# Kernel optimization log

Measured on AMD Instinct MI355X. Metric: run time of the kernel, lower is better.

## Reference

```python
import jax, jax.numpy as jnp
import numpy as np


def _conv_nchw(x, w, strides):
    # F.conv2d with padding=0 -> VALID, NCHW / OIHW layout
    return jax.lax.conv_general_dilated(
        x, w, window_strides=tuple(strides), padding="VALID",
        dimension_numbers=("NCHW", "OIHW", "NCHW"))


def setup_inputs() -> dict:
    key = jax.random.key(0)
    kx, kw, kb = jax.random.split(key, 3)
    # scale so values span the full int8 range and all 8 bit-planes are active
    x = jax.random.normal(kx, (64, 64, 56, 56), dtype=jnp.float32) * 60.0
    weight = jax.random.normal(kw, (128, 64, 3, 3), dtype=jnp.float32) * 0.05
    bias = jax.random.normal(kb, (128,), dtype=jnp.float32)
    return {"x": x, "weight": weight, "bias": bias}


def reference(x, weight, bias):
    strides = (1, 1)
    # clamp to int8 range and cast (torch.clamp + .type(torch.int8))
    xi = jnp.clip(x, -128, 127).astype(jnp.int8)
    y = jnp.zeros((), dtype=weight.dtype)
    for i in range(8):
        # arithmetic shift on signed int8, matching torch semantics
        bit = ((xi >> i) & 1).astype(weight.dtype)
        yi = jnp.clip(_conv_nchw(bit, weight, strides), -1024, 1023)
        scale = jnp.asarray(-128.0 if i == 7 else float(2 ** i), dtype=weight.dtype)
        y = y + yi * scale
    y = y + bias.reshape(1, -1, 1, 1)
    return y
```

## Files before the change

### kernel.cpp

```cpp
#include <hip/hip_runtime.h>
#include <stdint.h>

typedef unsigned short u16;
typedef __attribute__((ext_vector_type(8))) __bf16 bf16x8;
typedef __attribute__((ext_vector_type(4))) float f32x4;

#define N_IMG 64
#define C_IN  64
#define HW_IN 3136
#define W_IN  56
#define C_OUT 128
#define OH    54
#define OW    54
#define SPI   2916
#define KTOT  576
#define M_TOTAL (N_IMG*SPI)

typedef __attribute__((address_space(3))) unsigned int lds_uint;
typedef __attribute__((address_space(1))) unsigned int gbl_uint;

__device__ __forceinline__ void load16_to_lds(const u16* g, u16* l) {
  __builtin_amdgcn_global_load_lds((const gbl_uint*)g, (lds_uint*)l, 16, 0, 0);
}

__device__ inline u16 f32_bf16_rne(float f) {
  unsigned u = __float_as_uint(f);
  u = (u + 0x7FFFu + ((u >> 16) & 1u)) >> 16;
  return (u16)u;
}

__global__ void convert_w(const float* __restrict__ w, u16* __restrict__ wtT) {
  int o = blockIdx.x * 256 + threadIdx.x;
  if (o >= C_OUT * KTOT) return;
  int co = o / KTOT;
  int k  = o - co * KTOT;
  int t  = k >> 6;
  int ci = k & 63;
  wtT[o] = f32_bf16_rne(w[co * KTOT + ci * 9 + t]);
}

__global__ __launch_bounds__(256) void convert_x(const float* __restrict__ x,
                                                 u16* __restrict__ xt) {
  __shared__ u16 tile[64][66];
  int n  = blockIdx.y;
  int s0 = blockIdx.x * 64;
  int tx = threadIdx.x, ty = threadIdx.y;
  const float* xp = x + (size_t)n * C_IN * HW_IN;
  #pragma unroll
  for (int i = ty; i < 64; i += 4) {
    float v = xp[i * HW_IN + s0 + tx];
    v = fminf(fmaxf(v, -128.f), 127.f);
    int iv = (int)v;
    tile[i][tx] = f32_bf16_rne((float)iv);
  }
  __syncthreads();
  u16* op = xt + (size_t)n * HW_IN * C_IN;
  #pragma unroll
  for (int i = ty; i < 64; i += 4) {
    op[(size_t)(s0 + i) * C_IN + tx] = tile[tx][i];
  }
}

__global__ __launch_bounds__(256) void conv_gemm(
    const u16* __restrict__ xt, const u16* __restrict__ wtT,
    const float* __restrict__ bias, float* __restrict__ y)
{
  __shared__ u16 sP[128 * 64];
  __shared__ u16 sW[128 * 64];

  int tid  = threadIdx.x;
  int wv   = tid >> 6;
  int lane = tid & 63;
  int ln   = lane & 15;
  int q    = lane >> 4;
  int wy   = wv >> 1;
  int wx   = wv & 1;

  int blk_sp0 = blockIdx.x * 128;

  int r8 = lane >> 3;
  int cg = lane & 7;
  int scol = (cg ^ r8) * 8;

  int pix_off[4], wt_off[4];
  #pragma unroll
  for (int j = 0; j < 4; j++) {
    int srow = wv * 32 + j * 8 + r8;
    int p   = blk_sp0 + srow;
    int img = p / SPI;  int rem = p - img * SPI;
    int oh  = rem / OW; int ow  = rem - oh * OW;
    pix_off[j] = (img * HW_IN + oh * W_IN + ow) * C_IN + scol;
    wt_off[j]  = srow * KTOT + scol;
  }

  f32x4 acc[4][4];
  #pragma unroll
  for (int mt = 0; mt < 4; mt++)
    #pragma unroll
    for (int nt = 0; nt < 4; nt++)
      acc[mt][nt] = (f32x4){0.f, 0.f, 0.f, 0.f};

  int wrow[4], prow[4];
  #pragma unroll
  for (int i = 0; i < 4; i++) {
    wrow[i] = (wy * 64 + i * 16 + ln) * 64;
    prow[i] = (wx * 64 + i * 16 + ln) * 64;
  }
  int l7 = ln & 7;

  #pragma unroll
  for (int kc = 0; kc < 9; kc++) {
    int kh = kc / 3, kw = kc - kh * 3;
    int xoff = (kh * W_IN + kw) * C_IN;

    __syncthreads();
    #pragma unroll
    for (int j = 0; j < 4; j++)
      load16_to_lds(xt + pix_off[j] + xoff, sP + (wv * 32 + j * 8) * 64);
    #pragma unroll
    for (int j = 0; j < 4; j++)
      load16_to_lds(wtT + wt_off[j] + kc * 64, sW + (wv * 32 + j * 8) * 64);
    __syncthreads();

    #pragma unroll
    for (int s = 0; s < 2; s++) {
      int pg = ((s * 4 + q) ^ l7) * 8;
      bf16x8 wf[4], pf[4];
      #pragma unroll
      for (int mt = 0; mt < 4; mt++)
        wf[mt] = *(const bf16x8*)(sW + wrow[mt] + pg);
      #pragma unroll
      for (int nt = 0; nt < 4; nt++)
        pf[nt] = *(const bf16x8*)(sP + prow[nt] + pg);
      #pragma unroll
      for (int mt = 0; mt < 4; mt++)
        #pragma unroll
        for (int nt = 0; nt < 4; nt++)
          acc[mt][nt] = __builtin_amdgcn_mfma_f32_16x16x32_bf16(
              wf[mt], pf[nt], acc[mt][nt], 0, 0, 0);
    }
  }

  #pragma unroll
  for (int nt = 0; nt < 4; nt++) {
    int p   = blk_sp0 + wx * 64 + nt * 16 + ln;
    int img = p / SPI;  int rem = p - img * SPI;
    int oh  = rem / OW; int ow  = rem - oh * OW;
    int obase = img * C_OUT * SPI + oh * OW + ow;
    #pragma unroll
    for (int mt = 0; mt < 4; mt++) {
      int co0 = wy * 64 + mt * 16 + q * 4;
      #pragma unroll
      for (int r = 0; r < 4; r++) {
        int co = co0 + r;
        y[obase + co * SPI] = acc[mt][nt][r] + bias[co];
      }
    }
  }
}

extern "C" void kernel_launch(void* const* d_in, const int* in_sizes, int n_in,
                              void* d_out, int out_size, void* d_ws, size_t ws_size,
                              hipStream_t stream) {
  const float* x    = (const float*)d_in[0];
  const float* w    = (const float*)d_in[1];
  const float* bias = (const float*)d_in[2];
  float* y = (float*)d_out;

  u16* wtT = (u16*)d_ws;
  u16* xt  = (u16*)((char*)d_ws + (size_t)C_OUT * KTOT * sizeof(u16));

  hipLaunchKernelGGL(convert_w, dim3((C_OUT * KTOT + 255) / 256), dim3(256), 0, stream,
                     w, wtT);
  hipLaunchKernelGGL(convert_x, dim3(HW_IN / 64, N_IMG), dim3(64, 4), 0, stream,
                     x, xt);
  hipLaunchKernelGGL(conv_gemm, dim3(M_TOTAL / 128), dim3(256), 0, stream,
                     xt, wtT, bias, y);
}
```

Measured before the change: 187.3 us.

## Double-buffer LDS in conv GEMM, stage epilogue through LDS, merge convert kernels

The conv GEMM now double-buffers its LDS tiles so the global-to-LDS loads for the next filter tap are issued before the MFMAs on the current tap, leaving one barrier per iteration. The epilogue stages each wave's accumulators through LDS so that every store writes 64 consecutive output pixels per channel, making the large NCHW output write fully coalesced. The weight and input conversion kernels are merged into one launch, and the input transpose writes packed 32-bit pairs. In exchange, LDS use doubles, which may reduce occupancy. Correctness also relies on the async LDS loads being waited on before the single barrier.

```diff
diff --git a/kernel.cpp b/kernel.cpp
--- a/kernel.cpp
+++ b/kernel.cpp
@@ -2,6 +2,7 @@
 #include <stdint.h>
 
 typedef unsigned short u16;
+typedef unsigned int u32;
 typedef __attribute__((ext_vector_type(8))) __bf16 bf16x8;
 typedef __attribute__((ext_vector_type(4))) float f32x4;
 
@@ -29,35 +30,46 @@
   return (u16)u;
 }
 
-__global__ void convert_w(const float* __restrict__ w, u16* __restrict__ wtT) {
-  int o = blockIdx.x * 256 + threadIdx.x;
-  if (o >= C_OUT * KTOT) return;
-  int co = o / KTOT;
-  int k  = o - co * KTOT;
-  int t  = k >> 6;
-  int ci = k & 63;
-  wtT[o] = f32_bf16_rne(w[co * KTOT + ci * 9 + t]);
-}
-
-__global__ __launch_bounds__(256) void convert_x(const float* __restrict__ x,
-                                                 u16* __restrict__ xt) {
-  __shared__ u16 tile[64][66];
+__global__ __launch_bounds__(256) void convert_xw(const float* __restrict__ x,
+                                                  const float* __restrict__ w,
+                                                  u16* __restrict__ xt,
+                                                  u16* __restrict__ wtT) {
+  if (blockIdx.x == 49) {
+    int o = blockIdx.y * 256 + threadIdx.x;
+    #pragma unroll
+    for (int it = 0; it < 5; it++) {
+      int oo = o + it * 16384;
+      if (oo < C_OUT * KTOT) {
+        int co = oo / KTOT;
+        int k  = oo - co * KTOT;
+        int t2 = k >> 6, ci = k & 63;
+        wtT[oo] = f32_bf16_rne(w[co * KTOT + ci * 9 + t2]);
+      }
+    }
+    return;
+  }
+  __shared__ u16 tile[64][65];
+  int t  = threadIdx.x;
+  int tx = t & 63, ty = t >> 6;
   int n  = blockIdx.y;
   int s0 = blockIdx.x * 64;
-  int tx = threadIdx.x, ty = threadIdx.y;
-  const float* xp = x + (size_t)n * C_IN * HW_IN;
+  const float* xp = x + (size_t)n * C_IN * HW_IN + s0;
   #pragma unroll
   for (int i = ty; i < 64; i += 4) {
-    float v = xp[i * HW_IN + s0 + tx];
+    float v = xp[i * HW_IN + tx];
     v = fminf(fmaxf(v, -128.f), 127.f);
-    int iv = (int)v;
-    tile[i][tx] = f32_bf16_rne((float)iv);
+    v = truncf(v);
+    tile[i][tx] = (u16)(__float_as_uint(v) >> 16);
   }
   __syncthreads();
-  u16* op = xt + (size_t)n * HW_IN * C_IN;
+  u32* op = (u32*)(xt + (size_t)n * HW_IN * C_IN) + (size_t)s0 * 32;
   #pragma unroll
-  for (int i = ty; i < 64; i += 4) {
-    op[(size_t)(s0 + i) * C_IN + tx] = tile[tx][i];
+  for (int j = 0; j < 8; j++) {
+    int sp = j * 8 + ty * 2 + (tx >> 5);
+    int cp = tx & 31;
+    u32 lo = tile[2 * cp][sp];
+    u32 hi = tile[2 * cp + 1][sp];
+    op[sp * 32 + cp] = lo | (hi << 16);
   }
 }
 
@@ -65,8 +77,8 @@
     const u16* __restrict__ xt, const u16* __restrict__ wtT,
     const float* __restrict__ bias, float* __restrict__ y)
 {
-  __shared__ u16 sP[128 * 64];
-  __shared__ u16 sW[128 * 64];
+  __shared__ u16 sP[2][8192];
+  __shared__ u16 sW[2][8192];
 
   int tid  = threadIdx.x;
   int wv   = tid >> 6;
@@ -108,19 +120,25 @@
   }
   int l7 = ln & 7;
 
+#define STAGE(KC, BUF) do {                                                   \
+    int xoff_ = (((KC) / 3) * W_IN + ((KC) % 3)) * C_IN;                      \
+    _Pragma("unroll")                                                         \
+    for (int j_ = 0; j_ < 4; j_++)                                            \
+      load16_to_lds(xt + pix_off[j_] + xoff_,                                 \
+                    &sP[BUF][(wv * 32 + j_ * 8) * 64]);                       \
+    _Pragma("unroll")                                                         \
+    for (int j_ = 0; j_ < 4; j_++)                                            \
+      load16_to_lds(wtT + wt_off[j_] + (KC) * 64,                             \
+                    &sW[BUF][(wv * 32 + j_ * 8) * 64]);                       \
+  } while (0)
+
+  STAGE(0, 0);
+
   #pragma unroll
   for (int kc = 0; kc < 9; kc++) {
-    int kh = kc / 3, kw = kc - kh * 3;
-    int xoff = (kh * W_IN + kw) * C_IN;
-
+    int rb = kc & 1;
     __syncthreads();
-    #pragma unroll
-    for (int j = 0; j < 4; j++)
-      load16_to_lds(xt + pix_off[j] + xoff, sP + (wv * 32 + j * 8) * 64);
-    #pragma unroll
-    for (int j = 0; j < 4; j++)
-      load16_to_lds(wtT + wt_off[j] + kc * 64, sW + (wv * 32 + j * 8) * 64);
-    __syncthreads();
+    if (kc < 8) STAGE(kc + 1, rb ^ 1);
 
     #pragma unroll
     for (int s = 0; s < 2; s++) {
@@ -128,10 +146,10 @@
       bf16x8 wf[4], pf[4];
       #pragma unroll
       for (int mt = 0; mt < 4; mt++)
-        wf[mt] = *(const bf16x8*)(sW + wrow[mt] + pg);
+        wf[mt] = *(const bf16x8*)(&sW[rb][0] + wrow[mt] + pg);
       #pragma unroll
       for (int nt = 0; nt < 4; nt++)
-        pf[nt] = *(const bf16x8*)(sP + prow[nt] + pg);
+        pf[nt] = *(const bf16x8*)(&sP[rb][0] + prow[nt] + pg);
       #pragma unroll
       for (int mt = 0; mt < 4; mt++)
         #pragma unroll
@@ -140,21 +158,26 @@
               wf[mt], pf[nt], acc[mt][nt], 0, 0, 0);
     }
   }
+#undef STAGE
+
+  __syncthreads();
+  float* wbuf = ((float*)sP) + wv * (16 * 66);
+  int p   = blk_sp0 + wx * 64 + lane;
+  int img = p / SPI;  int rem = p - img * SPI;
+  size_t ybase = (size_t)img * C_OUT * SPI + rem;
 
   #pragma unroll
-  for (int nt = 0; nt < 4; nt++) {
-    int p   = blk_sp0 + wx * 64 + nt * 16 + ln;
-    int img = p / SPI;  int rem = p - img * SPI;
-    int oh  = rem / OW; int ow  = rem - oh * OW;
-    int obase = img * C_OUT * SPI + oh * OW + ow;
+  for (int mt = 0; mt < 4; mt++) {
     #pragma unroll
-    for (int mt = 0; mt < 4; mt++) {
-      int co0 = wy * 64 + mt * 16 + q * 4;
+    for (int nt = 0; nt < 4; nt++)
       #pragma unroll
-      for (int r = 0; r < 4; r++) {
-        int co = co0 + r;
-        y[obase + co * SPI] = acc[mt][nt][r] + bias[co];
-      }
+      for (int r = 0; r < 4; r++)
+        wbuf[(q * 4 + r) * 66 + nt * 16 + ln] = acc[mt][nt][r];
+    int co0 = wy * 64 + mt * 16;
+    #pragma unroll
+    for (int c = 0; c < 16; c++) {
+      float v = wbuf[c * 66 + lane] + bias[co0 + c];
+      y[ybase + (size_t)(co0 + c) * SPI] = v;
     }
   }
 }
@@ -170,10 +193,7 @@
   u16* wtT = (u16*)d_ws;
   u16* xt  = (u16*)((char*)d_ws + (size_t)C_OUT * KTOT * sizeof(u16));
 
-  hipLaunchKernelGGL(convert_w, dim3((C_OUT * KTOT + 255) / 256), dim3(256), 0, stream,
-                     w, wtT);
-  hipLaunchKernelGGL(convert_x, dim3(HW_IN / 64, N_IMG), dim3(64, 4), 0, stream,
-                     x, xt);
+  hipLaunchKernelGGL(convert_xw, dim3(50, 64), dim3(256), 0, stream, x, w, xt, wtT);
   hipLaunchKernelGGL(conv_gemm, dim3(M_TOTAL / 128), dim3(256), 0, stream,
                      xt, wtT, bias, y);
 }
```

New measurement: 194.4 us. 1.04x slower.
